# Performance work log

Hardware: AMD Instinct MI355X
Metric: run time of the kernel (lower is better)

## Reference

```python
import jax, jax.numpy as jnp
import numpy as np

VOCAB = 100000
EMB = 128
D = 8
K = 128
SUB = EMB // D  # 16
BN_EPS = 1e-3  # keras BatchNormalization default epsilon


def setup_inputs() -> dict:
    key = jax.random.key(0)
    k1, k2, k3 = jax.random.split(key, 3)
    ids = jax.random.randint(k1, (1024, 128), 0, VOCAB, dtype=jnp.int64)
    query_wemb = jax.random.normal(k2, (VOCAB, EMB), dtype=jnp.float32)
    centroids = jax.random.normal(k3, (D, K, SUB), dtype=jnp.float32)
    return {"ids": ids, "query_wemb": query_wemb, "centroids": centroids}


def reference(ids, query_wemb, centroids):
    d, k, sub = centroids.shape
    emb = d * sub
    flat = ids.reshape(-1)                      # [N]
    x = query_wemb[flat].reshape(-1, d, sub)    # [N, d, sub]

    norm_x = jnp.sum(x * x, axis=-1, keepdims=True)          # [N, d, 1]
    norm_c = jnp.sum(centroids * centroids, axis=-1)[None]   # [1, d, k]
    dot = jnp.einsum('nds,dks->ndk', x, centroids)           # [N, d, k]
    response = -norm_x + 2.0 * dot - norm_c                  # [N, d, k]

    # BatchNorm(scale=False, center=False), training=True: batch stats over
    # axes (0,1), per-k channel (keras default axis=-1)
    mean = jnp.mean(response, axis=(0, 1), keepdims=True)
    var = jnp.var(response, axis=(0, 1), keepdims=True)
    resp_bn = (response - mean) * jax.lax.rsqrt(var + BN_EPS)

    codes = jnp.argmax(resp_bn, axis=-1)                     # [N, d]

    # per-subspace centroid gather (non-shared centroids)
    outputs = centroids[jnp.arange(d)[None, :], codes]       # [N, d, sub]

    # straight-through estimator
    out_st = x + jax.lax.stop_gradient(outputs - x)          # [N, d, sub]
    return out_st.reshape(ids.shape + (emb,))
```

## Files before the change

kernel.cpp:

```cpp
#include <hip/hip_runtime.h>


constexpr int NTOK = 131072;
constexpr int ST   = 2320;
constexpr float EPS = 0.001f;

typedef float v2f __attribute__((ext_vector_type(2)));

__device__ inline float rlane(float v, int lane) {
    return __int_as_float(__builtin_amdgcn_readlane(__float_as_int(v), lane));
}


__global__ __launch_bounds__(256) void k1_stats(const int* __restrict__ ids,
                                                const float* __restrict__ wemb,
                                                float* __restrict__ partials,
                                                int tpb)
{
    __shared__ float xs[32][132];
    __shared__ float nrm[32][8];
    const int t = threadIdx.x;
    const int b = blockIdx.x;

    float g[4][4];
#pragma unroll
    for (int i = 0; i < 4; ++i)
#pragma unroll
        for (int j = 0; j < 4; ++j) g[i][j] = 0.f;
    float sx = 0.f, hh = 0.f, s2 = 0.f;

    const int d_g = t >> 4;
    const int r0  = ((t >> 2) & 3) << 2;
    const int c0  = (t & 3) << 2;
    const int u   = t & 127;
    const int d_s = u >> 4;
    const int s_s = u & 15;

    const int nchunks = tpb >> 5;
    for (int ch = 0; ch < nchunks; ++ch) {
        const int n0 = b * tpb + ch * 32;
#pragma unroll
        for (int rep = 0; rep < 4; ++rep) {
            int i = t + rep * 256;
            int n = i >> 5, f = i & 31;
            int id = ids[n0 + n];
            float4 v = *(const float4*)(wemb + (size_t)id * 128 + f * 4);
            *(float4*)(&xs[n][f * 4]) = v;
        }
        __syncthreads();
        {
            int n = t >> 3, dd = t & 7;
            const float* xp = &xs[n][dd * 16];
            float4 a = *(const float4*)(xp);
            float4 bq = *(const float4*)(xp + 4);
            float4 c = *(const float4*)(xp + 8);
            float4 dq = *(const float4*)(xp + 12);
            float acc = a.x*a.x + a.y*a.y + a.z*a.z + a.w*a.w;
            acc += bq.x*bq.x + bq.y*bq.y + bq.z*bq.z + bq.w*bq.w;
            acc += c.x*c.x + c.y*c.y + c.z*c.z + c.w*c.w;
            acc += dq.x*dq.x + dq.y*dq.y + dq.z*dq.z + dq.w*dq.w;
            nrm[n][dd] = acc;
        }
        __syncthreads();
        if (t < 128) {
            for (int n = 0; n < 32; ++n) {
                const float* xp = &xs[n][d_g * 16];
                float4 av = *(const float4*)(xp + r0);
                float4 bv = *(const float4*)(xp + c0);
                float aa[4] = {av.x, av.y, av.z, av.w};
                float bb[4] = {bv.x, bv.y, bv.z, bv.w};
#pragma unroll
                for (int i = 0; i < 4; ++i)
#pragma unroll
                    for (int j = 0; j < 4; ++j)
                        g[i][j] = fmaf(aa[i], bb[j], g[i][j]);
            }
        } else {
            for (int n = 0; n < 32; ++n) {
                float xv = xs[n][d_s * 16 + s_s];
                float nv = nrm[n][d_s];
                sx += xv;
                hh = fmaf(nv, xv, hh);
                if (s_s == 0) s2 = fmaf(nv, nv, s2);
            }
        }
        __syncthreads();
    }
    float* pb = partials + (size_t)b * ST;
    if (t < 128) {
        const int base = d_g * 256;
#pragma unroll
        for (int i = 0; i < 4; ++i)
#pragma unroll
            for (int j = 0; j < 4; ++j)
                pb[base + (r0 + i) * 16 + (c0 + j)] = g[i][j];
    } else {
        pb[2048 + d_s * 16 + s_s] = sx;
        pb[2176 + d_s * 16 + s_s] = hh;
        if (s_s == 0) pb[2304 + d_s] = s2;
    }
}

__global__ __launch_bounds__(256) void k2a_reduce(float* __restrict__ partials, int nb)
{
    const int idx = blockIdx.x * 256 + threadIdx.x;
    if (idx >= 2312) return;
    const int y = blockIdx.y;
    float acc[8] = {0.f, 0.f, 0.f, 0.f, 0.f, 0.f, 0.f, 0.f};
    int b = y;
    while (b + 7 * 32 < nb) {
#pragma unroll
        for (int u = 0; u < 8; ++u)
            acc[u] += partials[(size_t)(b + u * 32) * ST + idx];
        b += 8 * 32;
    }
    while (b < nb) { acc[0] += partials[(size_t)b * ST + idx]; b += 32; }
    float s = ((acc[0] + acc[1]) + (acc[2] + acc[3]))
            + ((acc[4] + acc[5]) + (acc[6] + acc[7]));
    partials[(size_t)y * ST + idx] = s;
}

__global__ __launch_bounds__(256) void k2b_reduce(const float* __restrict__ partials,
                                                  float* __restrict__ stats)
{
    const int idx = blockIdx.x * 256 + threadIdx.x;
    if (idx >= 2312) return;
    float acc[8] = {0.f, 0.f, 0.f, 0.f, 0.f, 0.f, 0.f, 0.f};
#pragma unroll
    for (int j = 0; j < 4; ++j)
#pragma unroll
        for (int u = 0; u < 8; ++u)
            acc[u] += partials[(size_t)(j * 8 + u) * ST + idx];
    stats[idx] = ((acc[0] + acc[1]) + (acc[2] + acc[3]))
               + ((acc[4] + acc[5]) + (acc[6] + acc[7]));
}

__global__ __launch_bounds__(128) void k3_final(const float* __restrict__ stats,
                                                const float* __restrict__ centroids,
                                                float2* __restrict__ ab)
{
    __shared__ float st[2312];
    const int t = threadIdx.x;
    for (int i = t; i < 2312; i += 128) st[i] = stats[i];
    __syncthreads();
    const int k = t;

    double Sn[8], Sn_tot = 0.0, S2_tot = 0.0;
#pragma unroll
    for (int d = 0; d < 8; ++d) {
        double s = 0.0;
        for (int ss = 0; ss < 16; ++ss) s += (double)st[d * 256 + ss * 17];
        Sn[d] = s; Sn_tot += s;
        S2_tot += (double)st[2304 + d];
    }
    double sr = -Sn_tot, sr2 = S2_tot;
    double ncd[8];
    for (int d = 0; d < 8; ++d) {
        const float* cp = centroids + d * 2048 + k * 16;
        float cv[16];
#pragma unroll
        for (int s = 0; s < 16; ++s) cv[s] = cp[s];
        double nc = 0, cdSx = 0, ch = 0, cGc = 0;
        for (int s = 0; s < 16; ++s) {
            nc   += (double)cv[s] * cv[s];
            cdSx += (double)cv[s] * st[2048 + d * 16 + s];
            ch   += (double)cv[s] * st[2176 + d * 16 + s];
            double rd = 0;
            for (int s2i = 0; s2i < 16; ++s2i)
                rd += (double)st[d * 256 + s * 16 + s2i] * cv[s2i];
            cGc += (double)cv[s] * rd;
        }
        ncd[d] = nc;
        sr  += 2.0 * cdSx - (double)NTOK * nc;
        sr2 += 4.0 * cGc + (double)NTOK * nc * nc + 2.0 * nc * Sn[d]
               - 4.0 * ch - 4.0 * nc * cdSx;
    }
    const double M = (double)NTOK * 8.0;
    double mean = sr / M;
    double var  = sr2 / M - mean * mean;
    float alpha = (float)(1.0 / sqrt(var + (double)EPS));
#pragma unroll
    for (int d = 0; d < 8; ++d) {
        float beta = (float)((double)alpha * (-ncd[d] - mean));
        ab[d * 128 + k] = make_float2(2.f * alpha, beta);
    }
}

__global__ __launch_bounds__(256, 4) void k4_main(const int* __restrict__ ids,
                                                  const float* __restrict__ wemb,
                                                  const float* __restrict__ centroids,
                                                  const float2* __restrict__ ab,
                                                  float* __restrict__ out)
{
    __shared__ __align__(16) float cs[128 * 16];

    const int t = threadIdx.x;
    const int d = blockIdx.y;
    const float* cd = centroids + (size_t)d * 2048;

#pragma unroll
    for (int i = 0; i < 2; ++i)
        ((float4*)cs)[t + i * 256] = ((const float4*)cd)[t + i * 256];

    const int lane = t & 63;
    const float2 g_lo = ab[(size_t)d * 128 + lane];
    const float2 g_hi = ab[(size_t)d * 128 + 64 + lane];

    const int nbase = blockIdx.x * 1024 + t;
    v2f x[4][8];
    float nx[4], best[4];
    int   code[4];
#pragma unroll
    for (int j = 0; j < 4; ++j) {
        const int n = nbase + j * 256;
        const float* xp = wemb + (size_t)ids[n] * 128 + d * 16;
        float s = 0.f;
#pragma unroll
        for (int q = 0; q < 4; ++q) {
            float4 v = *(const float4*)(xp + q * 4);
            x[j][q * 2]     = (v2f){v.x, v.y};
            x[j][q * 2 + 1] = (v2f){v.z, v.w};
            s += v.x * v.x + v.y * v.y + v.z * v.z + v.w * v.w;
        }
        nx[j] = -0.5f * s;
        best[j] = -3.4e38f;
        code[j] = 0;
    }

    __syncthreads();

    const unsigned cs_base = (unsigned)(unsigned long long)(const void*)&cs[0];

    float4 A0 = *(const float4*)(&cs[0]);
    float4 A1 = *(const float4*)(&cs[4]);
    float4 A2 = *(const float4*)(&cs[8]);
    float4 A3 = *(const float4*)(&cs[12]);
    float4 B0, B1, B2, B3;

#define COMPUTE(R0, R1, R2, R3, KK)                                          \
    {                                                                        \
        const int kk_ = (KK);                                                \
        const int kl_ = kk_ & 63;                                            \
        const float ga_ = rlane(kk_ < 64 ? g_lo.x : g_hi.x, kl_);            \
        const float gb_ = rlane(kk_ < 64 ? g_lo.y : g_hi.y, kl_);            \
        const v2f cc0 = (v2f){R0.x, R0.y}, cc1 = (v2f){R0.z, R0.w};          \
        const v2f cc2 = (v2f){R1.x, R1.y}, cc3 = (v2f){R1.z, R1.w};          \
        const v2f cc4 = (v2f){R2.x, R2.y}, cc5 = (v2f){R2.z, R2.w};          \
        const v2f cc6 = (v2f){R3.x, R3.y}, cc7 = (v2f){R3.z, R3.w};          \
        _Pragma("unroll")                                                    \
        for (int j = 0; j < 4; ++j) {                                        \
            v2f a = __builtin_elementwise_fma(cc0, x[j][0], (v2f){0.f,0.f}); \
            a = __builtin_elementwise_fma(cc1, x[j][1], a);                  \
            a = __builtin_elementwise_fma(cc2, x[j][2], a);                  \
            a = __builtin_elementwise_fma(cc3, x[j][3], a);                  \
            a = __builtin_elementwise_fma(cc4, x[j][4], a);                  \
            a = __builtin_elementwise_fma(cc5, x[j][5], a);                  \
            a = __builtin_elementwise_fma(cc6, x[j][6], a);                  \
            a = __builtin_elementwise_fma(cc7, x[j][7], a);                  \
            float acc = (a[0] + a[1]) + nx[j];                               \
            float sc = fmaf(ga_, acc, gb_);                                  \
            bool p = sc > best[j];             \
            best[j] = p ? sc : best[j];                                      \
            code[j] = p ? kk_ : code[j];                                     \
        }                                                                    \
    }

#define ISSUE(R0, R1, R2, R3, KK)                                            \
    {                                                                        \
        const unsigned ra_ = cs_base + (unsigned)(((KK) & 127) * 64);        \
        asm volatile("ds_read_b128 %0, %1"           : "=v"(R0) : "v"(ra_)); \
        asm volatile("ds_read_b128 %0, %1 offset:16" : "=v"(R1) : "v"(ra_)); \
        asm volatile("ds_read_b128 %0, %1 offset:32" : "=v"(R2) : "v"(ra_)); \
        asm volatile("ds_read_b128 %0, %1 offset:48" : "=v"(R3) : "v"(ra_)); \
    }

#define DRAIN()                                                              \
    __builtin_amdgcn_sched_barrier(0);                                       \
    asm volatile("s_waitcnt lgkmcnt(0)");                                    \
    __builtin_amdgcn_sched_barrier(0);

#pragma unroll 1
    for (int k = 0; k < 128; k += 2) {
        ISSUE(B0, B1, B2, B3, k + 1)
        COMPUTE(A0, A1, A2, A3, k)
        DRAIN()
        ISSUE(A0, A1, A2, A3, k + 2)
        COMPUTE(B0, B1, B2, B3, k + 1)
        DRAIN()
    }
#undef COMPUTE
#undef ISSUE
#undef DRAIN

#pragma unroll
    for (int j = 0; j < 4; ++j) {
        const int n = nbase + j * 256;
        const float* cw = cd + code[j] * 16;
        float* op = out + (size_t)n * 128 + d * 16;
#pragma unroll
        for (int q = 0; q < 4; ++q) {
            float4 cv = *(const float4*)(cw + q * 4);
            float x0 = x[j][q * 2][0],     x1 = x[j][q * 2][1];
            float x2 = x[j][q * 2 + 1][0], x3 = x[j][q * 2 + 1][1];
            float4 o;
            o.x = x0 + (cv.x - x0);
            o.y = x1 + (cv.y - x1);
            o.z = x2 + (cv.z - x2);
            o.w = x3 + (cv.w - x3);
            *(float4*)(op + q * 4) = o;
        }
    }
}

extern "C" void kernel_launch(void* const* d_in, const int* in_sizes, int n_in,
                              void* d_out, int out_size, void* d_ws, size_t ws_size,
                              hipStream_t stream)
{
    const int* ids    = (const int*)d_in[0];
    const float* wemb = (const float*)d_in[1];
    const float* cent = (const float*)d_in[2];
    float* out = (float*)d_out;
    float* ws  = (float*)d_ws;

    int p1b = 1024;
    if (ws_size < ((size_t)1024 * ST + 2320 + 2048) * 4) p1b = 512;
    if (ws_size < ((size_t)512  * ST + 2320 + 2048) * 4) p1b = 256;
    if (ws_size < ((size_t)256  * ST + 2320 + 2048) * 4) p1b = 128;
    const int tpb = NTOK / p1b;

    float* partials = ws;
    float* stats    = ws + (size_t)p1b * ST;
    float2* ab      = (float2*)(stats + 2320);

    hipLaunchKernelGGL(k1_stats,   dim3(p1b),     dim3(256), 0, stream, ids, wemb, partials, tpb);
    hipLaunchKernelGGL(k2a_reduce, dim3(10, 32),  dim3(256), 0, stream, partials, p1b);
    hipLaunchKernelGGL(k2b_reduce, dim3(10),      dim3(256), 0, stream, partials, stats);
    hipLaunchKernelGGL(k3_final,   dim3(1),       dim3(128), 0, stream, stats, cent, ab);
    hipLaunchKernelGGL(k4_main,    dim3(128, 8),  dim3(256), 0, stream, ids, wemb, cent, ab, out);
}
```

Before: 129.2 us.

## Double-buffer stats kernel gather and fold norm into FMA accumulator

The stats kernel now uses double-buffered shared tiles and prefetches the next chunk's embedding rows into registers while the current chunk is processed. The norm computation moves into the stat threads' branch, which removes one barrier per chunk. In the assignment kernel, the -0.5*||x||^2 term seeds the packed FMA accumulator instead of being added afterwards, saving one add per centroid per token. An extra sched_barrier is added after the LDS read issue. The costs are more register and LDS use, plus slightly different floating-point summation order.

```diff
diff --git a/kernel.cpp b/kernel.cpp
--- a/kernel.cpp
+++ b/kernel.cpp
@@ -17,7 +17,7 @@
                                                 float* __restrict__ partials,
                                                 int tpb)
 {
-    __shared__ float xs[32][132];
+    __shared__ float xs[2][32][132];
     __shared__ float nrm[32][8];
     const int t = threadIdx.x;
     const int b = blockIdx.x;
@@ -35,36 +35,34 @@
     const int u   = t & 127;
     const int d_s = u >> 4;
     const int s_s = u & 15;
+    const int ln[4] = { (t + 0) >> 5, (t + 256) >> 5, (t + 512) >> 5, (t + 768) >> 5 };
+    const int lf[4] = { (t + 0) & 31, (t + 256) & 31, (t + 512) & 31, (t + 768) & 31 };
 
     const int nchunks = tpb >> 5;
+    float4 v[4];
+
+    {
+        const int n0 = b * tpb;
+#pragma unroll
+        for (int rep = 0; rep < 4; ++rep)
+            v[rep] = *(const float4*)(wemb + (size_t)ids[n0 + ln[rep]] * 128 + lf[rep] * 4);
+#pragma unroll
+        for (int rep = 0; rep < 4; ++rep)
+            *(float4*)(&xs[0][ln[rep]][lf[rep] * 4]) = v[rep];
+    }
+
     for (int ch = 0; ch < nchunks; ++ch) {
-        const int n0 = b * tpb + ch * 32;
-#pragma unroll
-        for (int rep = 0; rep < 4; ++rep) {
-            int i = t + rep * 256;
-            int n = i >> 5, f = i & 31;
-            int id = ids[n0 + n];
-            float4 v = *(const float4*)(wemb + (size_t)id * 128 + f * 4);
-            *(float4*)(&xs[n][f * 4]) = v;
-        }
+        const int cur = ch & 1;
         __syncthreads();
-        {
-            int n = t >> 3, dd = t & 7;
-            const float* xp = &xs[n][dd * 16];
-            float4 a = *(const float4*)(xp);
-            float4 bq = *(const float4*)(xp + 4);
-            float4 c = *(const float4*)(xp + 8);
-            float4 dq = *(const float4*)(xp + 12);
-            float acc = a.x*a.x + a.y*a.y + a.z*a.z + a.w*a.w;
-            acc += bq.x*bq.x + bq.y*bq.y + bq.z*bq.z + bq.w*bq.w;
-            acc += c.x*c.x + c.y*c.y + c.z*c.z + c.w*c.w;
-            acc += dq.x*dq.x + dq.y*dq.y + dq.z*dq.z + dq.w*dq.w;
-            nrm[n][dd] = acc;
-        }
-        __syncthreads();
+        if (ch + 1 < nchunks) {
+            const int n0 = b * tpb + (ch + 1) * 32;
+#pragma unroll
+            for (int rep = 0; rep < 4; ++rep)
+                v[rep] = *(const float4*)(wemb + (size_t)ids[n0 + ln[rep]] * 128 + lf[rep] * 4);
+        }
         if (t < 128) {
             for (int n = 0; n < 32; ++n) {
-                const float* xp = &xs[n][d_g * 16];
+                const float* xp = &xs[cur][n][d_g * 16];
                 float4 av = *(const float4*)(xp + r0);
                 float4 bv = *(const float4*)(xp + c0);
                 float aa[4] = {av.x, av.y, av.z, av.w};
@@ -76,16 +74,33 @@
                         g[i][j] = fmaf(aa[i], bb[j], g[i][j]);
             }
         } else {
+#pragma unroll
+            for (int rep = 0; rep < 2; ++rep) {
+                const int tau = u + rep * 128;
+                const int n = tau >> 3, dd = tau & 7;
+                const float* xp = &xs[cur][n][dd * 16];
+                float acc = 0.f;
+#pragma unroll
+                for (int q = 0; q < 16; ++q) acc = fmaf(xp[q], xp[q], acc);
+                nrm[n][dd] = acc;
+            }
+            for (int n = 0; n < 32; ++n) sx += xs[cur][n][d_s * 16 + s_s];
+        }
+        if (ch + 1 < nchunks) {
+#pragma unroll
+            for (int rep = 0; rep < 4; ++rep)
+                *(float4*)(&xs[cur ^ 1][ln[rep]][lf[rep] * 4]) = v[rep];
+        }
+        __syncthreads();
+        if (t >= 128) {
             for (int n = 0; n < 32; ++n) {
-                float xv = xs[n][d_s * 16 + s_s];
                 float nv = nrm[n][d_s];
-                sx += xv;
-                hh = fmaf(nv, xv, hh);
+                hh = fmaf(nv, xs[cur][n][d_s * 16 + s_s], hh);
                 if (s_s == 0) s2 = fmaf(nv, nv, s2);
             }
         }
-        __syncthreads();
-    }
+    }
+
     float* pb = partials + (size_t)b * ST;
     if (t < 128) {
         const int base = d_g * 256;
@@ -208,7 +223,8 @@
 
     const int nbase = blockIdx.x * 1024 + t;
     v2f x[4][8];
-    float nx[4], best[4];
+    v2f nxv[4];
+    float best[4];
     int   code[4];
 #pragma unroll
     for (int j = 0; j < 4; ++j) {
@@ -222,7 +238,7 @@
             x[j][q * 2 + 1] = (v2f){v.z, v.w};
             s += v.x * v.x + v.y * v.y + v.z * v.z + v.w * v.w;
         }
-        nx[j] = -0.5f * s;
+        nxv[j] = (v2f){-0.5f * s, 0.f};
         best[j] = -3.4e38f;
         code[j] = 0;
     }
@@ -249,7 +265,7 @@
         const v2f cc6 = (v2f){R3.x, R3.y}, cc7 = (v2f){R3.z, R3.w};          \
         _Pragma("unroll")                                                    \
         for (int j = 0; j < 4; ++j) {                                        \
-            v2f a = __builtin_elementwise_fma(cc0, x[j][0], (v2f){0.f,0.f}); \
+            v2f a = __builtin_elementwise_fma(cc0, x[j][0], nxv[j]);         \
             a = __builtin_elementwise_fma(cc1, x[j][1], a);                  \
             a = __builtin_elementwise_fma(cc2, x[j][2], a);                  \
             a = __builtin_elementwise_fma(cc3, x[j][3], a);                  \
@@ -257,7 +273,7 @@
             a = __builtin_elementwise_fma(cc5, x[j][5], a);                  \
             a = __builtin_elementwise_fma(cc6, x[j][6], a);                  \
             a = __builtin_elementwise_fma(cc7, x[j][7], a);                  \
-            float acc = (a[0] + a[1]) + nx[j];                               \
+            float acc = a[0] + a[1];                                         \
             float sc = fmaf(ga_, acc, gb_);                                  \
             bool p = sc > best[j];             \
             best[j] = p ? sc : best[j];                                      \
@@ -272,10 +288,11 @@
         asm volatile("ds_read_b128 %0, %1 offset:16" : "=v"(R1) : "v"(ra_)); \
         asm volatile("ds_read_b128 %0, %1 offset:32" : "=v"(R2) : "v"(ra_)); \
         asm volatile("ds_read_b128 %0, %1 offset:48" : "=v"(R3) : "v"(ra_)); \
-    }
+    }                                                                        \
+    __builtin_amdgcn_sched_barrier(0);
 
 #define DRAIN()                                                              \
-    __builtin_amdgcn_sched_barrier(0);                                       \
+    __builtin_amdgcn_sched_barrier(0);        \
     asm volatile("s_waitcnt lgkmcnt(0)");                                    \
     __builtin_amdgcn_sched_barrier(0);
 
```

New measurement: 153.6 us. 18.9% more time.
